# Optimization experiments

Hardware: AMD Instinct MI355X
Metric: run time of the kernel (lower is better)

Reference implementation:

```python
import jax, jax.numpy as jnp
import numpy as np

N_NODES = 100000
SIG_DIM = 64
N_ADJ = 1600000
N_QUERY = 262144


def setup_inputs() -> dict:
    key = jax.random.key(0)
    k1, k2, k3, k4, k5 = jax.random.split(key, 5)
    x = jax.random.normal(k1, (N_NODES, SIG_DIM), dtype=jnp.float32)
    x = x / jnp.linalg.norm(x, axis=1, keepdims=True)  # F.normalize(p=2, dim=1)
    node_weight = jax.random.uniform(k2, (N_NODES,), dtype=jnp.float32)
    edges = jax.random.randint(k3, (2, N_QUERY), 0, N_NODES)
    adj_row = jnp.sort(jax.random.randint(k4, (N_ADJ,), 0, N_NODES))
    adj_col = jax.random.randint(k5, (N_ADJ,), 0, N_NODES)
    return {
        "x": x,
        "node_weight": node_weight,
        "edges": edges,
        "adj_row": adj_row,
        "adj_col": adj_col,
        "num_nodes": N_NODES,
    }


def reference(x, node_weight, edges, adj_row, adj_col, num_nodes):
    # node signatures scaled by node weight
    xw = x * node_weight[:, None]                      # [N, D]

    seg = lambda vals: jax.ops.segment_sum(vals, adj_row, num_segments=num_nodes)

    # SpMM propagation: (A @ x)[i] = sum_{j in N(i)} x[j]
    one_hop = seg(xw[adj_col])                          # [N, D]
    deg = seg(jnp.ones_like(adj_row, dtype=xw.dtype))   # [N]
    two_iter = seg(one_hop[adj_col])                    # [N, D]

    # combine mode
    two_hop = two_iter - one_hop - xw
    deg2 = jnp.maximum(seg(deg[adj_col]) - deg - 1.0, 0.0)

    row, col = edges[0], edges[1]
    x_u_1 = one_hop[row]
    x_v_1 = one_hop[col]
    x_u_2 = two_hop[row]
    x_v_2 = two_hop[col]

    dot = lambda a, b: (a * b).sum(axis=-1)

    deg_u = deg[row]
    deg_v = deg[col]
    deg_u_2 = deg2[row]
    deg_v_2 = deg2[col]

    count_1_1 = dot(x_u_1, x_v_1)
    count_1_2 = dot(x_u_1, x_v_2)
    count_2_1 = dot(x_u_2, x_v_1)
    count_2_2 = dot(x_u_2, x_v_2)
    count_1_inf = deg_u + deg_v - 2 * count_1_1 - count_1_2 - count_2_1
    count_2_inf = deg_u_2 + deg_v_2 - 2 * count_2_2 - count_1_2 - count_2_1

    x_u_iter = two_iter[row]
    x_v_iter = two_iter[col]
    x_u = xw[row]
    x_v = xw[col]
    comb_count_1_2 = dot(x_u_1, x_v_iter)
    comb_count_2_1 = dot(x_u_iter, x_v_1)
    comb_count_2_2 = dot(x_u_iter - deg_u[:, None] * x_u,
                         x_v_iter - deg_v[:, None] * x_v)
    comb_count_self_1_2 = dot(x_u_1, x_u_iter)
    comb_count_self_2_1 = dot(x_v_1, x_v_iter)

    features = jnp.stack([
        count_1_1, count_1_2, count_2_1, count_2_2,
        count_1_inf, count_2_inf,
        comb_count_1_2, comb_count_2_1, comb_count_2_2,
        comb_count_self_1_2, comb_count_self_2_1,
        deg_u, deg_v, deg_u_2, deg_v_2,
    ], axis=1)                                          # [E, 15]
    return features
```

## Files before the change

kernel.cpp:

```cpp
#include <hip/hip_runtime.h>


#define D 64

typedef unsigned int uint32;

__device__ __forceinline__ uint32 pack2(float a, float b) {
    uint32 ua = __float_as_uint(a);
    ua += 0x7fffu + ((ua >> 16) & 1u);
    uint32 ub = __float_as_uint(b);
    ub += 0x7fffu + ((ub >> 16) & 1u);
    return (ua >> 16) | (ub & 0xffff0000u);
}
__device__ __forceinline__ float lo2f(uint32 u) { return __uint_as_float(u << 16); }
__device__ __forceinline__ float hi2f(uint32 u) { return __uint_as_float(u & 0xffff0000u); }

#define RED_SLOT(v) { v += __shfl_xor(v, 8, 64); v += __shfl_xor(v, 16, 64); v += __shfl_xor(v, 32, 64); }
#define RED_GRP(v)  { v += __shfl_xor(v, 1, 64); v += __shfl_xor(v, 2, 64);  v += __shfl_xor(v, 4, 64);  }

__global__ void __launch_bounds__(256) xw_kernel(const float4* __restrict__ x,
                                                 const float* __restrict__ w,
                                                 uint4* __restrict__ xw, int n8) {
    int i = blockIdx.x * blockDim.x + threadIdx.x;
    if (i >= n8) return;
    float s = w[i >> 3];
    float4 a = x[i * 2], b = x[i * 2 + 1];
    uint4 o;
    o.x = pack2(a.x * s, a.y * s);
    o.y = pack2(a.z * s, a.w * s);
    o.z = pack2(b.x * s, b.y * s);
    o.w = pack2(b.z * s, b.w * s);
    xw[i] = o;
}

__global__ void __launch_bounds__(256) row_ptr_kernel(const int* __restrict__ adj_row,
                                                      int* __restrict__ row_ptr,
                                                      int n, int nadj) {
    int i = blockIdx.x * blockDim.x + threadIdx.x;
    if (i > n) return;
    int lo = 0, hi = nadj;
    while (lo < hi) {
        int mid = (lo + hi) >> 1;
        if (adj_row[mid] < i) lo = mid + 1; else hi = mid;
    }
    row_ptr[i] = lo;
}

template <bool WITH_DEG2>
__global__ void __launch_bounds__(256) spmm_kernel(const uint4* __restrict__ src,
                                                   const int* __restrict__ row_ptr,
                                                   const int* __restrict__ adj_col,
                                                   const float* __restrict__ degin,
                                                   uint4* __restrict__ dst,
                                                   float* __restrict__ degout,
                                                   int n) {
    int node = blockIdx.x * 4 + (threadIdx.x >> 6);
    int lane = threadIdx.x & 63;
    int slot = lane >> 3, sub = lane & 7;
    if (node >= n) return;
    int start = row_ptr[node], end = row_ptr[node + 1];
    float a0 = 0.f, a1 = 0.f, a2 = 0.f, a3 = 0.f,
          a4 = 0.f, a5 = 0.f, a6 = 0.f, a7 = 0.f;
    float dsum = 0.f;
    for (int base = start; base < end; base += 8) {
        int e = base + slot;
        bool valid = e < end;
        int ec = valid ? e : end - 1;
        int c = adj_col[ec];
        uint4 qv = src[c * 8 + sub];
        if (!valid) { qv.x = 0u; qv.y = 0u; qv.z = 0u; qv.w = 0u; }
        a0 += lo2f(qv.x); a1 += hi2f(qv.x);
        a2 += lo2f(qv.y); a3 += hi2f(qv.y);
        a4 += lo2f(qv.z); a5 += hi2f(qv.z);
        a6 += lo2f(qv.w); a7 += hi2f(qv.w);
        if (WITH_DEG2) dsum += valid ? degin[c] : 0.f;
    }
    RED_SLOT(a0) RED_SLOT(a1) RED_SLOT(a2) RED_SLOT(a3)
    RED_SLOT(a4) RED_SLOT(a5) RED_SLOT(a6) RED_SLOT(a7)
    if (WITH_DEG2) RED_SLOT(dsum)
    if (slot == 0) {
        uint4 o;
        o.x = pack2(a0, a1); o.y = pack2(a2, a3);
        o.z = pack2(a4, a5); o.w = pack2(a6, a7);
        dst[node * 8 + sub] = o;
    }
    if (lane == 0) {
        float dg = (float)(end - start);
        if (WITH_DEG2) degout[node] = fmaxf(dsum - dg - 1.0f, 0.0f);
        else           degout[node] = dg;
    }
}

__global__ void __launch_bounds__(256) edge_kernel(const int* __restrict__ edges,
                                                   const uint4* __restrict__ xw,
                                                   const uint4* __restrict__ h1,
                                                   const uint4* __restrict__ t2,
                                                   const float* __restrict__ deg,
                                                   const float* __restrict__ deg2,
                                                   float* __restrict__ out,
                                                   int E) {
    int t = blockIdx.x * blockDim.x + threadIdx.x;
    int q = t >> 3, sub = t & 7;
    if (q >= E) return;
    int u = edges[q], v = edges[E + q];
    uint4 pxu = xw[u * 8 + sub], pxv = xw[v * 8 + sub];
    uint4 phu = h1[u * 8 + sub], phv = h1[v * 8 + sub];
    uint4 ptu = t2[u * 8 + sub], ptv = t2[v * 8 + sub];
    float du = deg[u], dv = deg[v];

    float c11 = 0.f, c12 = 0.f, c21 = 0.f, c22 = 0.f,
          cc12 = 0.f, cc21 = 0.f, cc22 = 0.f, cs12 = 0.f, cs21 = 0.f;

    uint32 axu[4] = {pxu.x, pxu.y, pxu.z, pxu.w};
    uint32 axv[4] = {pxv.x, pxv.y, pxv.z, pxv.w};
    uint32 ahu[4] = {phu.x, phu.y, phu.z, phu.w};
    uint32 ahv[4] = {phv.x, phv.y, phv.z, phv.w};
    uint32 atu[4] = {ptu.x, ptu.y, ptu.z, ptu.w};
    uint32 atv[4] = {ptv.x, ptv.y, ptv.z, ptv.w};

    auto accum = [&](float xu, float xv, float hu, float hv, float tu, float tv) {
        float h2u = tu - hu - xu, h2v = tv - hv - xv;
        float au = fmaf(-du, xu, tu), av = fmaf(-dv, xv, tv);
        c11  = fmaf(hu,  hv,  c11);
        c12  = fmaf(hu,  h2v, c12);
        c21  = fmaf(h2u, hv,  c21);
        c22  = fmaf(h2u, h2v, c22);
        cc12 = fmaf(hu,  tv,  cc12);
        cc21 = fmaf(tu,  hv,  cc21);
        cc22 = fmaf(au,  av,  cc22);
        cs12 = fmaf(hu,  tu,  cs12);
        cs21 = fmaf(hv,  tv,  cs21);
    };
#pragma unroll
    for (int k = 0; k < 4; ++k) {
        accum(lo2f(axu[k]), lo2f(axv[k]), lo2f(ahu[k]), lo2f(ahv[k]), lo2f(atu[k]), lo2f(atv[k]));
        accum(hi2f(axu[k]), hi2f(axv[k]), hi2f(ahu[k]), hi2f(ahv[k]), hi2f(atu[k]), hi2f(atv[k]));
    }
    RED_GRP(c11) RED_GRP(c12) RED_GRP(c21) RED_GRP(c22)
    RED_GRP(cc12) RED_GRP(cc21) RED_GRP(cc22) RED_GRP(cs12) RED_GRP(cs21)

    if (sub == 0) {
        float du2 = deg2[u], dv2 = deg2[v];
        float* o = out + (size_t)q * 15;
        o[0]  = c11;
        o[1]  = c12;
        o[2]  = c21;
        o[3]  = c22;
        o[4]  = du + dv - 2.f * c11 - c12 - c21;
        o[5]  = du2 + dv2 - 2.f * c22 - c12 - c21;
        o[6]  = cc12;
        o[7]  = cc21;
        o[8]  = cc22;
        o[9]  = cs12;
        o[10] = cs21;
        o[11] = du;
        o[12] = dv;
        o[13] = du2;
        o[14] = dv2;
    }
}

extern "C" void kernel_launch(void* const* d_in, const int* in_sizes, int n_in,
                              void* d_out, int out_size, void* d_ws, size_t ws_size,
                              hipStream_t stream) {
    const float* x       = (const float*)d_in[0];
    const float* w       = (const float*)d_in[1];
    const int*   edges   = (const int*)d_in[2];
    const int*   adj_row = (const int*)d_in[3];
    const int*   adj_col = (const int*)d_in[4];

    const int N    = in_sizes[1];
    const int E    = in_sizes[2] / 2;
    const int NADJ = in_sizes[3];

    char* ws = (char*)d_ws;
    size_t off = 0;
    auto take = [&](size_t bytes) {
        void* p = ws + off;
        off = (off + bytes + 255) & ~(size_t)255;
        return p;
    };
    uint4* xw      = (uint4*)take((size_t)N * D * 2);
    uint4* one_hop = (uint4*)take((size_t)N * D * 2);
    uint4* two_it  = (uint4*)take((size_t)N * D * 2);
    float* deg     = (float*)take((size_t)N * sizeof(float));
    float* deg2    = (float*)take((size_t)N * sizeof(float));
    int*   row_ptr = (int*)take((size_t)(N + 1) * sizeof(int));
    (void)ws_size;

    float* out = (float*)d_out;

    {
        int n8 = N * 8;
        xw_kernel<<<(n8 + 255) / 256, 256, 0, stream>>>((const float4*)x, w, xw, n8);
    }
    row_ptr_kernel<<<(N + 1 + 255) / 256, 256, 0, stream>>>(adj_row, row_ptr, N, NADJ);
    spmm_kernel<false><<<(N + 3) / 4, 256, 0, stream>>>(xw, row_ptr, adj_col, nullptr,
                                                        one_hop, deg, N);
    spmm_kernel<true><<<(N + 3) / 4, 256, 0, stream>>>(one_hop, row_ptr, adj_col, deg,
                                                       two_it, deg2, N);
    edge_kernel<<<((size_t)E * 8 + 255) / 256, 256, 0, stream>>>(edges, xw, one_hop, two_it,
                                                                 deg, deg2, out, E);
}
```

Baseline: 215.4 us.

## Interleave node feature tables into one bundle and batch adjacency index loads

Stores xw, one_hop and two_iter for each node contiguously in a 384-byte bundle, and packs deg and deg2 into one float2. The edge kernel then reads all per-node data from one region instead of three separate tables. The SpMM kernel now loads 64 column indices per wave at once and broadcasts them with shuffles, replacing one index load per 8-edge step. The deg2 neighbour sum is spread across all lanes. In exchange, the SpMM gathers now stride through the larger bundle, which may hurt cache locality for the source table.

```diff
diff --git a/kernel.cpp b/kernel.cpp
--- a/kernel.cpp
+++ b/kernel.cpp
@@ -2,6 +2,10 @@
 
 
 #define D 64
+#define BSTRIDE 24
+#define XW_OFF 0
+#define H1_OFF 8
+#define T2_OFF 16
 
 typedef unsigned int uint32;
 
@@ -17,20 +21,22 @@
 
 #define RED_SLOT(v) { v += __shfl_xor(v, 8, 64); v += __shfl_xor(v, 16, 64); v += __shfl_xor(v, 32, 64); }
 #define RED_GRP(v)  { v += __shfl_xor(v, 1, 64); v += __shfl_xor(v, 2, 64);  v += __shfl_xor(v, 4, 64);  }
+#define RED_ALL(v)  { RED_GRP(v) RED_SLOT(v) }
 
 __global__ void __launch_bounds__(256) xw_kernel(const float4* __restrict__ x,
                                                  const float* __restrict__ w,
-                                                 uint4* __restrict__ xw, int n8) {
+                                                 uint4* __restrict__ bundle, int n8) {
     int i = blockIdx.x * blockDim.x + threadIdx.x;
     if (i >= n8) return;
-    float s = w[i >> 3];
+    int node = i >> 3, sub = i & 7;
+    float s = w[node];
     float4 a = x[i * 2], b = x[i * 2 + 1];
     uint4 o;
     o.x = pack2(a.x * s, a.y * s);
     o.y = pack2(a.z * s, a.w * s);
     o.z = pack2(b.x * s, b.y * s);
     o.w = pack2(b.z * s, b.w * s);
-    xw[i] = o;
+    bundle[(size_t)node * BSTRIDE + XW_OFF + sub] = o;
 }
 
 __global__ void __launch_bounds__(256) row_ptr_kernel(const int* __restrict__ adj_row,
@@ -50,63 +56,67 @@
 __global__ void __launch_bounds__(256) spmm_kernel(const uint4* __restrict__ src,
                                                    const int* __restrict__ row_ptr,
                                                    const int* __restrict__ adj_col,
-                                                   const float* __restrict__ degin,
+                                                   float2* __restrict__ degpair,
                                                    uint4* __restrict__ dst,
-                                                   float* __restrict__ degout,
                                                    int n) {
     int node = blockIdx.x * 4 + (threadIdx.x >> 6);
     int lane = threadIdx.x & 63;
     int slot = lane >> 3, sub = lane & 7;
     if (node >= n) return;
     int start = row_ptr[node], end = row_ptr[node + 1];
+    int deg_n = end - start;
     float a0 = 0.f, a1 = 0.f, a2 = 0.f, a3 = 0.f,
           a4 = 0.f, a5 = 0.f, a6 = 0.f, a7 = 0.f;
     float dsum = 0.f;
-    for (int base = start; base < end; base += 8) {
-        int e = base + slot;
-        bool valid = e < end;
-        int ec = valid ? e : end - 1;
-        int c = adj_col[ec];
-        uint4 qv = src[c * 8 + sub];
-        if (!valid) { qv.x = 0u; qv.y = 0u; qv.z = 0u; qv.w = 0u; }
-        a0 += lo2f(qv.x); a1 += hi2f(qv.x);
-        a2 += lo2f(qv.y); a3 += hi2f(qv.y);
-        a4 += lo2f(qv.z); a5 += hi2f(qv.z);
-        a6 += lo2f(qv.w); a7 += hi2f(qv.w);
-        if (WITH_DEG2) dsum += valid ? degin[c] : 0.f;
+    for (int base = 0; base < deg_n; base += 64) {
+        int cnt = deg_n - base; if (cnt > 64) cnt = 64;
+        int myc = adj_col[start + base + (lane < cnt ? lane : cnt - 1)];
+        if (WITH_DEG2) {
+            if (lane < cnt) dsum += degpair[myc].x;
+        }
+        for (int off = 0; off < cnt; off += 8) {
+            int e = off + slot;
+            int c = __shfl(myc, e, 64);
+            if (e < cnt) {
+                uint4 qv = src[(size_t)c * BSTRIDE + sub];
+                a0 += lo2f(qv.x); a1 += hi2f(qv.x);
+                a2 += lo2f(qv.y); a3 += hi2f(qv.y);
+                a4 += lo2f(qv.z); a5 += hi2f(qv.z);
+                a6 += lo2f(qv.w); a7 += hi2f(qv.w);
+            }
+        }
     }
     RED_SLOT(a0) RED_SLOT(a1) RED_SLOT(a2) RED_SLOT(a3)
     RED_SLOT(a4) RED_SLOT(a5) RED_SLOT(a6) RED_SLOT(a7)
-    if (WITH_DEG2) RED_SLOT(dsum)
+    if (WITH_DEG2) RED_ALL(dsum)
     if (slot == 0) {
         uint4 o;
         o.x = pack2(a0, a1); o.y = pack2(a2, a3);
         o.z = pack2(a4, a5); o.w = pack2(a6, a7);
-        dst[node * 8 + sub] = o;
+        dst[(size_t)node * BSTRIDE + sub] = o;
     }
     if (lane == 0) {
-        float dg = (float)(end - start);
-        if (WITH_DEG2) degout[node] = fmaxf(dsum - dg - 1.0f, 0.0f);
-        else           degout[node] = dg;
+        float* dp = (float*)&degpair[node];
+        if (WITH_DEG2) dp[1] = fmaxf(dsum - (float)deg_n - 1.0f, 0.0f);
+        else           dp[0] = (float)deg_n;
     }
 }
 
 __global__ void __launch_bounds__(256) edge_kernel(const int* __restrict__ edges,
-                                                   const uint4* __restrict__ xw,
-                                                   const uint4* __restrict__ h1,
-                                                   const uint4* __restrict__ t2,
-                                                   const float* __restrict__ deg,
-                                                   const float* __restrict__ deg2,
+                                                   const uint4* __restrict__ bundle,
+                                                   const float2* __restrict__ degpair,
                                                    float* __restrict__ out,
                                                    int E) {
     int t = blockIdx.x * blockDim.x + threadIdx.x;
     int q = t >> 3, sub = t & 7;
     if (q >= E) return;
     int u = edges[q], v = edges[E + q];
-    uint4 pxu = xw[u * 8 + sub], pxv = xw[v * 8 + sub];
-    uint4 phu = h1[u * 8 + sub], phv = h1[v * 8 + sub];
-    uint4 ptu = t2[u * 8 + sub], ptv = t2[v * 8 + sub];
-    float du = deg[u], dv = deg[v];
+    const uint4* bu = bundle + (size_t)u * BSTRIDE;
+    const uint4* bv = bundle + (size_t)v * BSTRIDE;
+    uint4 pxu = bu[XW_OFF + sub], phu = bu[H1_OFF + sub], ptu = bu[T2_OFF + sub];
+    uint4 pxv = bv[XW_OFF + sub], phv = bv[H1_OFF + sub], ptv = bv[T2_OFF + sub];
+    float2 dpu = degpair[u], dpv = degpair[v];
+    float du = dpu.x, du2 = dpu.y, dv = dpv.x, dv2 = dpv.y;
 
     float c11 = 0.f, c12 = 0.f, c21 = 0.f, c22 = 0.f,
           cc12 = 0.f, cc21 = 0.f, cc22 = 0.f, cs12 = 0.f, cs21 = 0.f;
@@ -140,7 +150,6 @@
     RED_GRP(cc12) RED_GRP(cc21) RED_GRP(cc22) RED_GRP(cs12) RED_GRP(cs21)
 
     if (sub == 0) {
-        float du2 = deg2[u], dv2 = deg2[v];
         float* o = out + (size_t)q * 15;
         o[0]  = c11;
         o[1]  = c12;
@@ -180,25 +189,21 @@
         off = (off + bytes + 255) & ~(size_t)255;
         return p;
     };
-    uint4* xw      = (uint4*)take((size_t)N * D * 2);
-    uint4* one_hop = (uint4*)take((size_t)N * D * 2);
-    uint4* two_it  = (uint4*)take((size_t)N * D * 2);
-    float* deg     = (float*)take((size_t)N * sizeof(float));
-    float* deg2    = (float*)take((size_t)N * sizeof(float));
-    int*   row_ptr = (int*)take((size_t)(N + 1) * sizeof(int));
+    uint4*  bundle  = (uint4*)take((size_t)N * BSTRIDE * sizeof(uint4));
+    float2* degpair = (float2*)take((size_t)N * sizeof(float2));
+    int*    row_ptr = (int*)take((size_t)(N + 1) * sizeof(int));
     (void)ws_size;
 
     float* out = (float*)d_out;
 
     {
         int n8 = N * 8;
-        xw_kernel<<<(n8 + 255) / 256, 256, 0, stream>>>((const float4*)x, w, xw, n8);
+        xw_kernel<<<(n8 + 255) / 256, 256, 0, stream>>>((const float4*)x, w, bundle, n8);
     }
     row_ptr_kernel<<<(N + 1 + 255) / 256, 256, 0, stream>>>(adj_row, row_ptr, N, NADJ);
-    spmm_kernel<false><<<(N + 3) / 4, 256, 0, stream>>>(xw, row_ptr, adj_col, nullptr,
-                                                        one_hop, deg, N);
-    spmm_kernel<true><<<(N + 3) / 4, 256, 0, stream>>>(one_hop, row_ptr, adj_col, deg,
-                                                       two_it, deg2, N);
-    edge_kernel<<<((size_t)E * 8 + 255) / 256, 256, 0, stream>>>(edges, xw, one_hop, two_it,
-                                                                 deg, deg2, out, E);
-}
+    spmm_kernel<false><<<(N + 3) / 4, 256, 0, stream>>>(bundle + XW_OFF, row_ptr, adj_col,
+                                                        degpair, bundle + H1_OFF, N);
+    spmm_kernel<true><<<(N + 3) / 4, 256, 0, stream>>>(bundle + H1_OFF, row_ptr, adj_col,
+                                                       degpair, bundle + T2_OFF, N);
+    edge_kernel<<<((size_t)E * 8 + 255) / 256, 256, 0, stream>>>(edges, bundle, degpair, out, E);
+}
```

Result: no change. 215.3 us (-0.1%).

## Assign one 8-lane group per node in SpMM with shuffled column indices

Applied to the files above, without the earlier changes.

The SpMM kernel now maps each node to an 8-lane group instead of a full 64-lane wavefront, so a wavefront handles 8 nodes and the launch grid shrinks accordingly. Column indices are loaded cooperatively and broadcast by shuffle, and each lane accumulates its 8-element slice serially over neighbours, which removes the cross-slot shuffle reduction. With average degree around 16, this is meant to avoid idle lanes and reduction overhead. In exchange, per-lane work becomes serial over the neighbour list, and degree imbalance between nodes sharing a wavefront causes divergence. Indexing is also widened to size_t.

```diff
diff --git a/kernel.cpp b/kernel.cpp
--- a/kernel.cpp
+++ b/kernel.cpp
@@ -15,7 +15,6 @@
 __device__ __forceinline__ float lo2f(uint32 u) { return __uint_as_float(u << 16); }
 __device__ __forceinline__ float hi2f(uint32 u) { return __uint_as_float(u & 0xffff0000u); }
 
-#define RED_SLOT(v) { v += __shfl_xor(v, 8, 64); v += __shfl_xor(v, 16, 64); v += __shfl_xor(v, 32, 64); }
 #define RED_GRP(v)  { v += __shfl_xor(v, 1, 64); v += __shfl_xor(v, 2, 64);  v += __shfl_xor(v, 4, 64);  }
 
 __global__ void __launch_bounds__(256) xw_kernel(const float4* __restrict__ x,
@@ -50,44 +49,46 @@
 __global__ void __launch_bounds__(256) spmm_kernel(const uint4* __restrict__ src,
                                                    const int* __restrict__ row_ptr,
                                                    const int* __restrict__ adj_col,
-                                                   const float* __restrict__ degin,
+                                                   const float* __restrict__ degv,
                                                    uint4* __restrict__ dst,
                                                    float* __restrict__ degout,
                                                    int n) {
-    int node = blockIdx.x * 4 + (threadIdx.x >> 6);
     int lane = threadIdx.x & 63;
-    int slot = lane >> 3, sub = lane & 7;
+    int g = lane >> 3, sub = lane & 7;
+    int node = blockIdx.x * 32 + (threadIdx.x >> 6) * 8 + g;
     if (node >= n) return;
     int start = row_ptr[node], end = row_ptr[node + 1];
+    int deg_n = end - start;
     float a0 = 0.f, a1 = 0.f, a2 = 0.f, a3 = 0.f,
           a4 = 0.f, a5 = 0.f, a6 = 0.f, a7 = 0.f;
     float dsum = 0.f;
-    for (int base = start; base < end; base += 8) {
-        int e = base + slot;
-        bool valid = e < end;
-        int ec = valid ? e : end - 1;
-        int c = adj_col[ec];
-        uint4 qv = src[c * 8 + sub];
-        if (!valid) { qv.x = 0u; qv.y = 0u; qv.z = 0u; qv.w = 0u; }
-        a0 += lo2f(qv.x); a1 += hi2f(qv.x);
-        a2 += lo2f(qv.y); a3 += hi2f(qv.y);
-        a4 += lo2f(qv.z); a5 += hi2f(qv.z);
-        a6 += lo2f(qv.w); a7 += hi2f(qv.w);
-        if (WITH_DEG2) dsum += valid ? degin[c] : 0.f;
-    }
-    RED_SLOT(a0) RED_SLOT(a1) RED_SLOT(a2) RED_SLOT(a3)
-    RED_SLOT(a4) RED_SLOT(a5) RED_SLOT(a6) RED_SLOT(a7)
-    if (WITH_DEG2) RED_SLOT(dsum)
-    if (slot == 0) {
-        uint4 o;
-        o.x = pack2(a0, a1); o.y = pack2(a2, a3);
-        o.z = pack2(a4, a5); o.w = pack2(a6, a7);
-        dst[node * 8 + sub] = o;
-    }
-    if (lane == 0) {
-        float dg = (float)(end - start);
-        if (WITH_DEG2) degout[node] = fmaxf(dsum - dg - 1.0f, 0.0f);
-        else           degout[node] = dg;
+    int gbase = lane & 56;
+    for (int base = 0; base < deg_n; base += 8) {
+        int k = base + sub;
+        bool kv = k < deg_n;
+        int idx = kv ? adj_col[start + k] : 0;
+        if (WITH_DEG2) { if (kv) dsum += degv[idx]; }
+#pragma unroll
+        for (int i = 0; i < 8; ++i) {
+            int c = __shfl(idx, gbase + i, 64);
+            if (base + i < deg_n) {
+                uint4 qv = src[(size_t)c * 8 + sub];
+                a0 += lo2f(qv.x); a1 += hi2f(qv.x);
+                a2 += lo2f(qv.y); a3 += hi2f(qv.y);
+                a4 += lo2f(qv.z); a5 += hi2f(qv.z);
+                a6 += lo2f(qv.w); a7 += hi2f(qv.w);
+            }
+        }
+    }
+    uint4 o;
+    o.x = pack2(a0, a1); o.y = pack2(a2, a3);
+    o.z = pack2(a4, a5); o.w = pack2(a6, a7);
+    dst[(size_t)node * 8 + sub] = o;
+    if (WITH_DEG2) {
+        RED_GRP(dsum)
+        if (sub == 0) degout[node] = fmaxf(dsum - (float)deg_n - 1.0f, 0.0f);
+    } else {
+        if (sub == 0) degout[node] = (float)deg_n;
     }
 }
 
@@ -103,9 +104,9 @@
     int q = t >> 3, sub = t & 7;
     if (q >= E) return;
     int u = edges[q], v = edges[E + q];
-    uint4 pxu = xw[u * 8 + sub], pxv = xw[v * 8 + sub];
-    uint4 phu = h1[u * 8 + sub], phv = h1[v * 8 + sub];
-    uint4 ptu = t2[u * 8 + sub], ptv = t2[v * 8 + sub];
+    uint4 pxu = xw[(size_t)u * 8 + sub], pxv = xw[(size_t)v * 8 + sub];
+    uint4 phu = h1[(size_t)u * 8 + sub], phv = h1[(size_t)v * 8 + sub];
+    uint4 ptu = t2[(size_t)u * 8 + sub], ptv = t2[(size_t)v * 8 + sub];
     float du = deg[u], dv = deg[v];
 
     float c11 = 0.f, c12 = 0.f, c21 = 0.f, c22 = 0.f,
@@ -195,10 +196,10 @@
         xw_kernel<<<(n8 + 255) / 256, 256, 0, stream>>>((const float4*)x, w, xw, n8);
     }
     row_ptr_kernel<<<(N + 1 + 255) / 256, 256, 0, stream>>>(adj_row, row_ptr, N, NADJ);
-    spmm_kernel<false><<<(N + 3) / 4, 256, 0, stream>>>(xw, row_ptr, adj_col, nullptr,
-                                                        one_hop, deg, N);
-    spmm_kernel<true><<<(N + 3) / 4, 256, 0, stream>>>(one_hop, row_ptr, adj_col, deg,
-                                                       two_it, deg2, N);
+    spmm_kernel<false><<<(N + 31) / 32, 256, 0, stream>>>(xw, row_ptr, adj_col, nullptr,
+                                                          one_hop, deg, N);
+    spmm_kernel<true><<<(N + 31) / 32, 256, 0, stream>>>(one_hop, row_ptr, adj_col, deg,
+                                                         two_it, deg2, N);
     edge_kernel<<<((size_t)E * 8 + 255) / 256, 256, 0, stream>>>(edges, xw, one_hop, two_it,
                                                                  deg, deg2, out, E);
 }
```

Measured after the change: 199.1 us. 7.6% less time.
